# Kernel optimization log

Hardware: AMD Instinct MI355X
Metric: run time of the kernel (lower is better)

## Reference

```python
import jax, jax.numpy as jnp
import numpy as np

HEADS = 16
ROPE_BASE = 10000.0


def _rope(x):
    # x: [B, S, D]; rotate interleaved even/odd pairs across full D
    B, S, D = x.shape
    half = D // 2
    inv_freq = 1.0 / (ROPE_BASE ** (jnp.arange(half, dtype=jnp.float32) * 2.0 / D))
    ang = jnp.arange(S, dtype=jnp.float32)[:, None] * inv_freq[None, :]  # [S, half]
    cos, sin = jnp.cos(ang), jnp.sin(ang)
    xp = x.reshape(B, S, half, 2)
    xe, xo = xp[..., 0], xp[..., 1]
    re = xe * cos - xo * sin
    ro = xe * sin + xo * cos
    return jnp.stack([re, ro], axis=-1).reshape(B, S, D)


def setup_inputs() -> dict:
    key = jax.random.key(0)
    ks = jax.random.split(key, 7)
    B, S, D = 2, 2048, 1024
    sc = 1.0 / np.sqrt(D)
    return {
        "queries": jax.random.normal(ks[0], (B, S, D), jnp.float32),
        "keys": jax.random.normal(ks[1], (B, S, D), jnp.float32),
        "values": jax.random.normal(ks[2], (B, S, D), jnp.float32),
        "Wq": jax.random.normal(ks[3], (D, D), jnp.float32) * sc,
        "Wk": jax.random.normal(ks[4], (D, D), jnp.float32) * sc,
        "Wv": jax.random.normal(ks[5], (D, D), jnp.float32) * sc,
        "Wo": jax.random.normal(ks[6], (D, D), jnp.float32) * sc,
    }


def reference(queries, keys, values, Wq, Wk, Wv, Wo):
    B, S, D = queries.shape
    H = HEADS
    dk = D // H
    # bias-free linear projections (torch Linear: x @ W^T)
    q = _rope(queries @ Wq.T)
    k = _rope(keys @ Wk.T)
    v = _rope(values @ Wv.T)
    # split heads: [B, H, S, dk]
    q = q.reshape(B, S, H, dk).transpose(0, 2, 1, 3)
    k = k.reshape(B, S, H, dk).transpose(0, 2, 1, 3)
    v = v.reshape(B, S, H, dk).transpose(0, 2, 1, 3)
    scores = jnp.einsum("bhqd,bhkd->bhqk", q, k) / jnp.sqrt(jnp.float32(dk))
    attn = jax.nn.softmax(scores, axis=-1)
    ctx = jnp.einsum("bhqk,bhkd->bhqd", attn, v)  # [B, H, S, dk]
    z = ctx.transpose(0, 2, 1, 3).reshape(B, S, D)
    return z @ Wo.T
```

## Files before the change

kernel.cpp:

```cpp
#include <hip/hip_runtime.h>
#include <hip/hip_bf16.h>
#include <math.h>


typedef __attribute__((ext_vector_type(8))) short s8v;
typedef __attribute__((ext_vector_type(8))) __bf16 bf16x8;
typedef __attribute__((ext_vector_type(4))) float f32x4;
typedef __attribute__((ext_vector_type(16))) float f32x16;
typedef __attribute__((ext_vector_type(2))) unsigned u32x2;

__device__ inline unsigned short f2bf(float f) {
    unsigned u = __builtin_bit_cast(unsigned, f);
    u += 0x7FFFu + ((u >> 16) & 1u);
    return (unsigned short)(u >> 16);
}

__device__ inline unsigned pk_bf16(float a, float b) {
    __hip_bfloat162 h = __float22bfloat162_rn(float2{a, b});
    unsigned u;
    __builtin_memcpy(&u, &h, 4);
    return u;
}

__device__ inline f32x4 mfma16(s8v a, s8v b, f32x4 c) {
    return __builtin_amdgcn_mfma_f32_16x16x32_bf16(
        __builtin_bit_cast(bf16x8, a), __builtin_bit_cast(bf16x8, b), c, 0, 0, 0);
}

__device__ inline f32x16 mfma32(s8v a, s8v b, f32x16 c) {
    return __builtin_amdgcn_mfma_f32_32x32x16_bf16(
        __builtin_bit_cast(bf16x8, a), __builtin_bit_cast(bf16x8, b), c, 0, 0, 0);
}

struct CvtArgs {
    const float* s[7];
    unsigned short* d[7];
    int n4[7];
};

__global__ __launch_bounds__(256) void cvt_kernel(CvtArgs a) {
    const int which = blockIdx.y;
    const float4* __restrict__ src = (const float4*)a.s[which];
    unsigned short* __restrict__ dst = a.d[which];
    const int n4 = a.n4[which];
    for (int i = blockIdx.x * 256 + threadIdx.x; i < n4; i += gridDim.x * 256) {
        float4 v = src[i];
        uint2 o;
        o.x = pk_bf16(v.x, v.y);
        o.y = pk_bf16(v.z, v.w);
        *(uint2*)(dst + (size_t)i * 4) = o;
    }
}

__global__ __launch_bounds__(256) void rope_table_kernel(float* __restrict__ cosT,
                                                         float* __restrict__ sinT) {
    int i = blockIdx.x * 256 + threadIdx.x;
    int s = i >> 9, d2 = i & 511;
    float inv = exp2f((float)d2 * (-13.287712379549449f / 512.0f));
    float ang = (float)s * inv;
    float sn, cs;
    sincosf(ang, &sn, &cs);
    cosT[i] = cs;
    sinT[i] = sn;
}

struct GemmArgs {
    const unsigned short* A[3];
    const unsigned short* W[3];
    void* C[3];
    const float* cosT;
    const float* sinT;
    float scale[3];
};

template <bool ROPE>
__global__ __launch_bounds__(256) void gemm_bt(GemmArgs g) {
    constexpr int K = 1024, N = 1024;
    const int z = blockIdx.z;
    const unsigned short* __restrict__ A = g.A[z];
    const unsigned short* __restrict__ W = g.W[z];

    const int tid = threadIdx.x;
    const int lane = tid & 63, wid = tid >> 6;
    const int wr = wid >> 1, wc = wid & 1;
    const int row0 = blockIdx.x * 128, col0 = blockIdx.y * 128;
    const int lr = lane & 15, kofs = (lane >> 4) * 8;

    __shared__ __align__(16) unsigned short As[128][72];
    __shared__ __align__(16) unsigned short Ws[128][72];

    f32x4 acc[4][4] = {};

    const int srow = tid >> 3;
    const int schunk = (tid & 7) * 8;

    for (int k0 = 0; k0 < K; k0 += 64) {
        __syncthreads();
#pragma unroll
        for (int i = 0; i < 4; ++i) {
            int r = srow + i * 32;
            *(s8v*)(&As[r][schunk]) =
                *(const s8v*)(A + (size_t)(row0 + r) * K + k0 + schunk);
            *(s8v*)(&Ws[r][schunk]) =
                *(const s8v*)(W + (size_t)(col0 + r) * K + k0 + schunk);
        }
        __syncthreads();

        s8v af[2][4], bf[2][4];
#pragma unroll
        for (int ks = 0; ks < 2; ++ks) {
#pragma unroll
            for (int m = 0; m < 4; ++m)
                af[ks][m] = *(const s8v*)(&As[wr * 64 + m * 16 + lr][ks * 32 + kofs]);
#pragma unroll
            for (int n = 0; n < 4; ++n)
                bf[ks][n] = *(const s8v*)(&Ws[wc * 64 + n * 16 + lr][ks * 32 + kofs]);
        }
#pragma unroll
        for (int m = 0; m < 4; ++m)
#pragma unroll
            for (int n = 0; n < 4; ++n) {
                acc[m][n] = mfma16(af[0][m], bf[0][n], acc[m][n]);
                acc[m][n] = mfma16(af[1][m], bf[1][n], acc[m][n]);
            }
    }

    const int rbase = row0 + wr * 64 + ((lane >> 4) << 2);
    const int cbase = col0 + wc * 64 + lr;
    const float scale = g.scale[z];
#pragma unroll
    for (int m = 0; m < 4; ++m) {
#pragma unroll
        for (int n = 0; n < 4; ++n) {
            const int gc = cbase + n * 16;
#pragma unroll
            for (int r = 0; r < 4; ++r) {
                const int gr = rbase + m * 16 + r;
                float v = acc[m][n][r];
                if constexpr (ROPE) {
                    const int s = gr & 2047;
                    const int d2 = gc >> 1;
                    float cs = g.cosT[s * 512 + d2];
                    float sn = g.sinT[s * 512 + d2];
                    float partner = __shfl_xor(v, 1);
                    v = (v * cs + partner * ((lane & 1) ? sn : -sn)) * scale;
                    ((unsigned short*)g.C[z])[(size_t)gr * N + gc] = f2bf(v);
                } else {
                    ((float*)g.C[z])[(size_t)gr * N + gc] = v;
                }
            }
        }
    }
}

__global__ __launch_bounds__(512, 2) void attn_kernel(
    const unsigned short* __restrict__ Q,
    const unsigned short* __restrict__ Km,
    const unsigned short* __restrict__ Vm,
    unsigned short* __restrict__ ctx) {
    const int tid = threadIdx.x;
    const int lane = tid & 63;
    const int w = tid >> 6;
    const int hi = lane >> 5;
    const int lq = lane & 31;
    const int qt = blockIdx.x;
    const int bh = blockIdx.y;
    const size_t base = (size_t)(bh >> 4) * 2048 * 1024;
    const int hcol = (bh & 15) * 64;
    const int q0 = qt * 256 + w * 32;

    __shared__ __align__(16) unsigned short Vt[2][64][72];

    const int vkey = tid >> 3;
    const int vc = tid & 7;
    const int vphys = ((((vkey >> 3) ^ vc) << 3) | (vkey & 7));

    auto stageV = [&](int buf, s8v vv) {
#pragma unroll
        for (int j = 0; j < 8; ++j)
            Vt[buf][vc * 8 + j][vphys] = (unsigned short)vv[j];
    };

    const unsigned short* __restrict__ Kp = Km + base + (size_t)lq * 1024 + hcol + hi * 8;
    const unsigned short* __restrict__ Vp = Vm + base + (size_t)vkey * 1024 + hcol + vc * 8;

    s8v qf[4];
#pragma unroll
    for (int s = 0; s < 4; ++s)
        qf[s] = *(const s8v*)(Q + base + (size_t)(q0 + lq) * 1024 + hcol + s * 16 + hi * 8);

    s8v kfA[8], kfB[8];
#pragma unroll
    for (int i = 0; i < 8; ++i)
        kfA[i] = *(const s8v*)(Kp + (size_t)((i >> 2) * 32) * 1024 + (i & 3) * 16);

    stageV(0, *(const s8v*)Vp);
    __syncthreads();

    f32x16 accO0 = {}, accO1 = {};
    float lacc = 0.f;

#define ATTN_STEP(KT, CUR, KFC, KFN)                                            \
    {                                                                           \
        const int kt_ = (KT);                                                   \
        const bool pre_ = (kt_ + 64 < 2048);                                    \
        s8v vnxt_;                                                              \
        if (pre_) {                                                             \
                               \
            vnxt_ = *(const s8v*)(Vp + (size_t)(kt_ + 64) * 1024);              \
            __builtin_amdgcn_sched_barrier(0);                                  \
            _Pragma("unroll")                                                   \
            for (int i = 0; i < 8; ++i)                                         \
                KFN[i] = *(const s8v*)(Kp +                                     \
                    (size_t)(kt_ + 64 + (i >> 2) * 32) * 1024 + (i & 3) * 16);  \
        }                                                                       \
                                       \
        f32x16 s0 = {}, s1 = {};                                                \
        __builtin_amdgcn_s_setprio(1);                                          \
        _Pragma("unroll")                                                       \
        for (int s = 0; s < 4; ++s) {                                           \
            s0 = mfma32(KFC[s], qf[s], s0);                                     \
            s1 = mfma32(KFC[4 + s], qf[s], s1);                                 \
        }                                                                       \
        __builtin_amdgcn_s_setprio(0);                                          \
                                 \
        s8v vf[8];                                                              \
        _Pragma("unroll")                                                       \
        for (int db = 0; db < 2; ++db)                                          \
            _Pragma("unroll")                                                   \
            for (int ks = 0; ks < 4; ++ks)                                      \
                vf[db * 4 + ks] = *(const s8v*)&Vt[CUR][db * 32 + lq]           \
                    [((2 * ks + hi) ^ ((db * 4 + (lq >> 3)) & 7)) << 3];        \
                                  \
        _Pragma("unroll")                                                       \
        for (int r = 0; r < 16; ++r) {                                          \
            s0[r] = exp2f(s0[r]);                                               \
            s1[r] = exp2f(s1[r]);                                               \
        }                                                                       \
        float t16[16];                                                          \
        _Pragma("unroll")                                                       \
        for (int r = 0; r < 16; ++r) t16[r] = s0[r] + s1[r];                    \
        _Pragma("unroll")                                                       \
        for (int r = 0; r < 8; ++r) t16[r] += t16[r + 8];                       \
        _Pragma("unroll")                                                       \
        for (int r = 0; r < 4; ++r) t16[r] += t16[r + 4];                       \
        lacc += (t16[0] + t16[1]) + (t16[2] + t16[3]);                          \
                                                 \
        unsigned w0[8], w1[8];                                                  \
        _Pragma("unroll")                                                       \
        for (int g = 0; g < 4; ++g) {                                           \
            const int rr = g * 4;                                               \
            w0[g] = pk_bf16(s0[rr], s0[rr + 1]);                                \
            w1[g] = pk_bf16(s0[rr + 2], s0[rr + 3]);                            \
        }                                                                       \
        _Pragma("unroll")                                                       \
        for (int g = 4; g < 8; ++g) {                                           \
            const int rr = (g - 4) * 4;                                         \
            w0[g] = pk_bf16(s1[rr], s1[rr + 1]);                                \
            w1[g] = pk_bf16(s1[rr + 2], s1[rr + 3]);                            \
        }                                                                       \
               \
        s8v pf[4];                                                              \
        _Pragma("unroll")                                                       \
        for (int ks = 0; ks < 4; ++ks) {                                        \
            int4 fi;                                                            \
            PK_SWAP(fi, w0[2 * ks], w0[2 * ks + 1], w1[2 * ks], w1[2 * ks + 1]);\
            pf[ks] = __builtin_bit_cast(s8v, fi);                               \
        }                                                                       \
         \
                          \
        if (pre_) stageV((CUR) ^ 1, vnxt_);                                     \
        asm volatile("s_waitcnt lgkmcnt(0)" ::: "memory");                      \
        __builtin_amdgcn_s_barrier();                                           \
        __builtin_amdgcn_sched_barrier(0);                                      \
                                                        \
        __builtin_amdgcn_s_setprio(1);                                          \
        _Pragma("unroll")                                                       \
        for (int ks = 0; ks < 4; ++ks) {                                        \
            accO0 = mfma32(vf[ks], pf[ks], accO0);                              \
            accO1 = mfma32(vf[4 + ks], pf[ks], accO1);                          \
        }                                                                       \
        __builtin_amdgcn_s_setprio(0);                                          \
    }

#if __has_builtin(__builtin_amdgcn_permlane32_swap)
#define PK_SWAP(fi, a0, b0, a1, b1)                                             \
    {                                                                           \
        u32x2 ra_ = __builtin_amdgcn_permlane32_swap((a0), (b0), false, false); \
        u32x2 rb_ = __builtin_amdgcn_permlane32_swap((a1), (b1), false, false); \
        fi.x = (int)ra_[0]; fi.y = (int)rb_[0];                                 \
        fi.z = (int)ra_[1]; fi.w = (int)rb_[1];                                 \
    }
#else
#define PK_SWAP(fi, a0, b0, a1, b1)                                             \
    {                                                                           \
        unsigned own0 = hi ? (b0) : (a0);                                       \
        unsigned own1 = hi ? (b1) : (a1);                                       \
        unsigned snd0 = hi ? (a0) : (b0);                                       \
        unsigned snd1 = hi ? (a1) : (b1);                                       \
        unsigned rcv0 = (unsigned)__shfl_xor((int)snd0, 32);                    \
        unsigned rcv1 = (unsigned)__shfl_xor((int)snd1, 32);                    \
        fi.x = (int)(hi ? rcv0 : own0);                                         \
        fi.y = (int)(hi ? rcv1 : own1);                                         \
        fi.z = (int)(hi ? own0 : rcv0);                                         \
        fi.w = (int)(hi ? own1 : rcv1);                                         \
    }
#endif

    for (int kt = 0; kt < 2048; kt += 128) {
        ATTN_STEP(kt, 0, kfA, kfB);
        ATTN_STEP(kt + 64, 1, kfB, kfA);
    }
#undef ATTN_STEP
#undef PK_SWAP

    const float ltot = lacc + __shfl_xor(lacc, 32);
    const float rl = 1.0f / ltot;
    unsigned short* dst = ctx + base + (size_t)(q0 + lq) * 1024 + hcol;
#pragma unroll
    for (int r = 0; r < 16; ++r) {
        const int d = (r & 3) + 8 * (r >> 2) + 4 * hi;
        dst[d] = f2bf(accO0[r] * rl);
        dst[d + 32] = f2bf(accO1[r] * rl);
    }
}

extern "C" void kernel_launch(void* const* d_in, const int* in_sizes, int n_in,
                              void* d_out, int out_size, void* d_ws, size_t ws_size,
                              hipStream_t stream) {
    char* ws = (char*)d_ws;
    size_t off = 0;
    auto alloc = [&](size_t bytes) {
        void* p = ws + off;
        off += (bytes + 255) & ~(size_t)255;
        return p;
    };

    const size_t XB = (size_t)4096 * 1024 * 2;
    const size_t WB = (size_t)1024 * 1024 * 2;
    const size_t TB = (size_t)2048 * 512 * 4;

    unsigned short* Xb[3];
    for (int i = 0; i < 3; ++i) Xb[i] = (unsigned short*)alloc(XB);
    unsigned short* Wb[4];
    for (int i = 0; i < 4; ++i) Wb[i] = (unsigned short*)alloc(WB);
    unsigned short* Qb = (unsigned short*)alloc(XB);
    unsigned short* Kb = (unsigned short*)alloc(XB);
    unsigned short* Vb = (unsigned short*)alloc(XB);
    float* cosT = (float*)alloc(TB);
    float* sinT = (float*)alloc(TB);
    unsigned short* ctx = Xb[0];

    CvtArgs ca;
    unsigned short* dsts[7] = {Xb[0], Xb[1], Xb[2], Wb[0], Wb[1], Wb[2], Wb[3]};
    for (int i = 0; i < 7; ++i) {
        ca.s[i] = (const float*)d_in[i];
        ca.d[i] = dsts[i];
        ca.n4[i] = in_sizes[i] / 4;
    }
    cvt_kernel<<<dim3(1024, 7), 256, 0, stream>>>(ca);

    rope_table_kernel<<<4096, 256, 0, stream>>>(cosT, sinT);

    GemmArgs gp;
    gp.A[0] = Xb[0]; gp.A[1] = Xb[1]; gp.A[2] = Xb[2];
    gp.W[0] = Wb[0]; gp.W[1] = Wb[1]; gp.W[2] = Wb[2];
    gp.C[0] = Qb;    gp.C[1] = Kb;    gp.C[2] = Vb;
    gp.cosT = cosT;  gp.sinT = sinT;
    gp.scale[0] = 0.125f * 1.4426950408889634f;
    gp.scale[1] = 1.0f;
    gp.scale[2] = 1.0f;
    gemm_bt<true><<<dim3(32, 8, 3), 256, 0, stream>>>(gp);

    attn_kernel<<<dim3(8, 32), 512, 0, stream>>>(Qb, Kb, Vb, ctx);

    GemmArgs go;
    go.A[0] = ctx;   go.A[1] = ctx;   go.A[2] = ctx;
    go.W[0] = Wb[3]; go.W[1] = Wb[3]; go.W[2] = Wb[3];
    go.C[0] = d_out; go.C[1] = d_out; go.C[2] = d_out;
    go.cosT = cosT;  go.sinT = sinT;
    go.scale[0] = 1.0f; go.scale[1] = 1.0f; go.scale[2] = 1.0f;
    gemm_bt<false><<<dim3(32, 8, 1), 256, 0, stream>>>(go);
}
```

Baseline: 180.7 us.

## Split attention over two KV halves and add a combine kernel

Each attention block now processes only half of the key/value sequence, doubling the grid to 512 blocks to fill more compute units. Unnormalized fp32 partial outputs and row sums are written to workspace, and a new combine kernel adds the halves, normalizes and converts to bf16. The block index is remapped to interleave work across the chip. This costs extra global memory traffic for the fp32 partials and an additional kernel launch.

```diff
diff --git a/kernel.cpp b/kernel.cpp
--- a/kernel.cpp
+++ b/kernel.cpp
@@ -157,17 +157,23 @@
     const unsigned short* __restrict__ Q,
     const unsigned short* __restrict__ Km,
     const unsigned short* __restrict__ Vm,
-    unsigned short* __restrict__ ctx) {
+    float* __restrict__ Op,
+    float* __restrict__ Lp) {
     const int tid = threadIdx.x;
     const int lane = tid & 63;
     const int w = tid >> 6;
     const int hi = lane >> 5;
     const int lq = lane & 31;
-    const int qt = blockIdx.x;
-    const int bh = blockIdx.y;
+    const int flat = blockIdx.x;
+    const int vid = (flat & 7) * 64 + (flat >> 3);
+    const int qt = vid & 7;
+    const int bh = (vid >> 3) & 31;
+    const int half = vid >> 8;
     const size_t base = (size_t)(bh >> 4) * 2048 * 1024;
     const int hcol = (bh & 15) * 64;
     const int q0 = qt * 256 + w * 32;
+    const int kv0 = half * 1024;
+    const int kend = kv0 + 1024;
 
     __shared__ __align__(16) unsigned short Vt[2][64][72];
 
@@ -192,9 +198,9 @@
     s8v kfA[8], kfB[8];
 #pragma unroll
     for (int i = 0; i < 8; ++i)
-        kfA[i] = *(const s8v*)(Kp + (size_t)((i >> 2) * 32) * 1024 + (i & 3) * 16);
-
-    stageV(0, *(const s8v*)Vp);
+        kfA[i] = *(const s8v*)(Kp + (size_t)(kv0 + (i >> 2) * 32) * 1024 + (i & 3) * 16);
+
+    stageV(0, *(const s8v*)(Vp + (size_t)kv0 * 1024));
     __syncthreads();
 
     f32x16 accO0 = {}, accO1 = {};
@@ -203,7 +209,7 @@
 #define ATTN_STEP(KT, CUR, KFC, KFN)                                            \
     {                                                                           \
         const int kt_ = (KT);                                                   \
-        const bool pre_ = (kt_ + 64 < 2048);                                    \
+        const bool pre_ = (kt_ + 64 < kend);                                    \
         s8v vnxt_;                                                              \
         if (pre_) {                                                             \
                                \
@@ -267,8 +273,8 @@
             PK_SWAP(fi, w0[2 * ks], w0[2 * ks + 1], w1[2 * ks], w1[2 * ks + 1]);\
             pf[ks] = __builtin_bit_cast(s8v, fi);                               \
         }                                                                       \
-         \
-                          \
+           \
+                      \
         if (pre_) stageV((CUR) ^ 1, vnxt_);                                     \
         asm volatile("s_waitcnt lgkmcnt(0)" ::: "memory");                      \
         __builtin_amdgcn_s_barrier();                                           \
@@ -307,22 +313,43 @@
     }
 #endif
 
-    for (int kt = 0; kt < 2048; kt += 128) {
+    for (int kt = kv0; kt < kend; kt += 128) {
         ATTN_STEP(kt, 0, kfA, kfB);
         ATTN_STEP(kt + 64, 1, kfB, kfA);
     }
 #undef ATTN_STEP
 #undef PK_SWAP
 
+    const int grow = (bh >> 4) * 2048 + q0 + lq;
+    float* dst = Op + ((size_t)half * 4096 + grow) * 1024 + hcol;
+#pragma unroll
+    for (int g = 0; g < 4; ++g) {
+        float4 v0 = make_float4(accO0[g * 4], accO0[g * 4 + 1],
+                                accO0[g * 4 + 2], accO0[g * 4 + 3]);
+        float4 v1 = make_float4(accO1[g * 4], accO1[g * 4 + 1],
+                                accO1[g * 4 + 2], accO1[g * 4 + 3]);
+        *(float4*)(dst + g * 8 + 4 * hi) = v0;
+        *(float4*)(dst + 32 + g * 8 + 4 * hi) = v1;
+    }
     const float ltot = lacc + __shfl_xor(lacc, 32);
-    const float rl = 1.0f / ltot;
-    unsigned short* dst = ctx + base + (size_t)(q0 + lq) * 1024 + hcol;
-#pragma unroll
-    for (int r = 0; r < 16; ++r) {
-        const int d = (r & 3) + 8 * (r >> 2) + 4 * hi;
-        dst[d] = f2bf(accO0[r] * rl);
-        dst[d + 32] = f2bf(accO1[r] * rl);
-    }
+    if (!hi) Lp[((size_t)half * 4096 + grow) * 16 + (bh & 15)] = ltot;
+}
+
+__global__ __launch_bounds__(256) void combine_kernel(const float* __restrict__ Op,
+                                                      const float* __restrict__ Lp,
+                                                      unsigned short* __restrict__ ctx) {
+    const int i = blockIdx.x * 256 + threadIdx.x;
+    const int row = i >> 8;
+    const int h = (i & 255) >> 4;
+    const float l = Lp[row * 16 + h] + Lp[4096 * 16 + row * 16 + h];
+    const float rl = 1.0f / l;
+    const float4* p = (const float4*)Op;
+    float4 a = p[i];
+    float4 b = p[(4096 * 1024 / 4) + i];
+    uint2 o;
+    o.x = pk_bf16((a.x + b.x) * rl, (a.y + b.y) * rl);
+    o.y = pk_bf16((a.z + b.z) * rl, (a.w + b.w) * rl);
+    *(uint2*)(ctx + (size_t)i * 4) = o;
 }
 
 extern "C" void kernel_launch(void* const* d_in, const int* in_sizes, int n_in,
@@ -349,6 +376,8 @@
     unsigned short* Vb = (unsigned short*)alloc(XB);
     float* cosT = (float*)alloc(TB);
     float* sinT = (float*)alloc(TB);
+    float* Op = (float*)alloc((size_t)2 * 4096 * 1024 * 4);
+    float* Lp = (float*)alloc((size_t)2 * 4096 * 16 * 4);
     unsigned short* ctx = Xb[0];
 
     CvtArgs ca;
@@ -372,7 +401,9 @@
     gp.scale[2] = 1.0f;
     gemm_bt<true><<<dim3(32, 8, 3), 256, 0, stream>>>(gp);
 
-    attn_kernel<<<dim3(8, 32), 512, 0, stream>>>(Qb, Kb, Vb, ctx);
+    attn_kernel<<<512, 512, 0, stream>>>(Qb, Kb, Vb, Op, Lp);
+
+    combine_kernel<<<4096, 256, 0, stream>>>(Op, Lp, ctx);
 
     GemmArgs go;
     go.A[0] = ctx;   go.A[1] = ctx;   go.A[2] = ctx;
```

Measured after the change: 190.1 us. 1.05x slower.

## Software-pipeline QK scores one tile ahead and remap attention block order

Applied to the files above, without the earlier changes.

Restructures the attention loop so the QK^T MFMA for the next key tile runs before the exp/softmax and PV of the current tile, with score accumulators ping-ponged and K fragments prefetched two tiles ahead. The V tile in shared memory goes from a 2-deep to a 4-deep ring, and the XOR swizzle is replaced by a padded row stride of 66. The grid is flattened and remapped so that consecutive blocks cover different heads rather than the same head. The aim is to overlap matrix-core work with the exp and pack work and to improve L2 locality. The cost is more live registers, and the unswizzled padded layout may bring back LDS bank conflicts.

```diff
diff --git a/kernel.cpp b/kernel.cpp
--- a/kernel.cpp
+++ b/kernel.cpp
@@ -163,26 +163,22 @@
     const int w = tid >> 6;
     const int hi = lane >> 5;
     const int lq = lane & 31;
-    const int qt = blockIdx.x;
-    const int bh = blockIdx.y;
+    const int flat = blockIdx.x;
+    const int vid = (flat & 7) * 32 + (flat >> 3);
+    const int qt = vid & 7;
+    const int bh = vid >> 3;
     const size_t base = (size_t)(bh >> 4) * 2048 * 1024;
     const int hcol = (bh & 15) * 64;
     const int q0 = qt * 256 + w * 32;
 
-    __shared__ __align__(16) unsigned short Vt[2][64][72];
+    __shared__ __align__(16) unsigned short Vt[4][64][66];
 
     const int vkey = tid >> 3;
     const int vc = tid & 7;
-    const int vphys = ((((vkey >> 3) ^ vc) << 3) | (vkey & 7));
-
-    auto stageV = [&](int buf, s8v vv) {
-#pragma unroll
-        for (int j = 0; j < 8; ++j)
-            Vt[buf][vc * 8 + j][vphys] = (unsigned short)vv[j];
-    };
-
-    const unsigned short* __restrict__ Kp = Km + base + (size_t)lq * 1024 + hcol + hi * 8;
-    const unsigned short* __restrict__ Vp = Vm + base + (size_t)vkey * 1024 + hcol + vc * 8;
+
+    const unsigned short* kpa = Km + base + (size_t)lq * 1024 + hcol + hi * 8;
+    const unsigned short* kpb = kpa + 32 * 1024;
+    const unsigned short* vst = Vm + base + (size_t)vkey * 1024 + hcol + vc * 8;
 
     s8v qf[4];
 #pragma unroll
@@ -192,96 +188,28 @@
     s8v kfA[8], kfB[8];
 #pragma unroll
     for (int i = 0; i < 8; ++i)
-        kfA[i] = *(const s8v*)(Kp + (size_t)((i >> 2) * 32) * 1024 + (i & 3) * 16);
-
-    stageV(0, *(const s8v*)Vp);
+        kfA[i] = *(const s8v*)(((i >> 2) ? kpb : kpa) + (i & 3) * 16);
+    {
+        s8v v0 = *(const s8v*)vst;
+#pragma unroll
+        for (int j = 0; j < 8; ++j) Vt[0][vc * 8 + j][vkey] = (unsigned short)v0[j];
+    }
+#pragma unroll
+    for (int i = 0; i < 8; ++i)
+        kfB[i] = *(const s8v*)(((i >> 2) ? kpb : kpa) + 65536 + (i & 3) * 16);
+    f32x16 scA0 = {}, scA1 = {}, scB0 = {}, scB1 = {};
+#pragma unroll
+    for (int s = 0; s < 4; ++s) {
+        scA0 = mfma32(kfA[s], qf[s], scA0);
+        scA1 = mfma32(kfA[4 + s], qf[s], scA1);
+    }
+    kpa += 2 * 65536;
+    kpb += 2 * 65536;
+    vst += 65536;
     __syncthreads();
 
     f32x16 accO0 = {}, accO1 = {};
     float lacc = 0.f;
-
-#define ATTN_STEP(KT, CUR, KFC, KFN)                                            \
-    {                                                                           \
-        const int kt_ = (KT);                                                   \
-        const bool pre_ = (kt_ + 64 < 2048);                                    \
-        s8v vnxt_;                                                              \
-        if (pre_) {                                                             \
-                               \
-            vnxt_ = *(const s8v*)(Vp + (size_t)(kt_ + 64) * 1024);              \
-            __builtin_amdgcn_sched_barrier(0);                                  \
-            _Pragma("unroll")                                                   \
-            for (int i = 0; i < 8; ++i)                                         \
-                KFN[i] = *(const s8v*)(Kp +                                     \
-                    (size_t)(kt_ + 64 + (i >> 2) * 32) * 1024 + (i & 3) * 16);  \
-        }                                                                       \
-                                       \
-        f32x16 s0 = {}, s1 = {};                                                \
-        __builtin_amdgcn_s_setprio(1);                                          \
-        _Pragma("unroll")                                                       \
-        for (int s = 0; s < 4; ++s) {                                           \
-            s0 = mfma32(KFC[s], qf[s], s0);                                     \
-            s1 = mfma32(KFC[4 + s], qf[s], s1);                                 \
-        }                                                                       \
-        __builtin_amdgcn_s_setprio(0);                                          \
-                                 \
-        s8v vf[8];                                                              \
-        _Pragma("unroll")                                                       \
-        for (int db = 0; db < 2; ++db)                                          \
-            _Pragma("unroll")                                                   \
-            for (int ks = 0; ks < 4; ++ks)                                      \
-                vf[db * 4 + ks] = *(const s8v*)&Vt[CUR][db * 32 + lq]           \
-                    [((2 * ks + hi) ^ ((db * 4 + (lq >> 3)) & 7)) << 3];        \
-                                  \
-        _Pragma("unroll")                                                       \
-        for (int r = 0; r < 16; ++r) {                                          \
-            s0[r] = exp2f(s0[r]);                                               \
-            s1[r] = exp2f(s1[r]);                                               \
-        }                                                                       \
-        float t16[16];                                                          \
-        _Pragma("unroll")                                                       \
-        for (int r = 0; r < 16; ++r) t16[r] = s0[r] + s1[r];                    \
-        _Pragma("unroll")                                                       \
-        for (int r = 0; r < 8; ++r) t16[r] += t16[r + 8];                       \
-        _Pragma("unroll")                                                       \
-        for (int r = 0; r < 4; ++r) t16[r] += t16[r + 4];                       \
-        lacc += (t16[0] + t16[1]) + (t16[2] + t16[3]);                          \
-                                                 \
-        unsigned w0[8], w1[8];                                                  \
-        _Pragma("unroll")                                                       \
-        for (int g = 0; g < 4; ++g) {                                           \
-            const int rr = g * 4;                                               \
-            w0[g] = pk_bf16(s0[rr], s0[rr + 1]);                                \
-            w1[g] = pk_bf16(s0[rr + 2], s0[rr + 3]);                            \
-        }                                                                       \
-        _Pragma("unroll")                                                       \
-        for (int g = 4; g < 8; ++g) {                                           \
-            const int rr = (g - 4) * 4;                                         \
-            w0[g] = pk_bf16(s1[rr], s1[rr + 1]);                                \
-            w1[g] = pk_bf16(s1[rr + 2], s1[rr + 3]);                            \
-        }                                                                       \
-               \
-        s8v pf[4];                                                              \
-        _Pragma("unroll")                                                       \
-        for (int ks = 0; ks < 4; ++ks) {                                        \
-            int4 fi;                                                            \
-            PK_SWAP(fi, w0[2 * ks], w0[2 * ks + 1], w1[2 * ks], w1[2 * ks + 1]);\
-            pf[ks] = __builtin_bit_cast(s8v, fi);                               \
-        }                                                                       \
-         \
-                          \
-        if (pre_) stageV((CUR) ^ 1, vnxt_);                                     \
-        asm volatile("s_waitcnt lgkmcnt(0)" ::: "memory");                      \
-        __builtin_amdgcn_s_barrier();                                           \
-        __builtin_amdgcn_sched_barrier(0);                                      \
-                                                        \
-        __builtin_amdgcn_s_setprio(1);                                          \
-        _Pragma("unroll")                                                       \
-        for (int ks = 0; ks < 4; ++ks) {                                        \
-            accO0 = mfma32(vf[ks], pf[ks], accO0);                              \
-            accO1 = mfma32(vf[4 + ks], pf[ks], accO1);                          \
-        }                                                                       \
-        __builtin_amdgcn_s_setprio(0);                                          \
-    }
 
 #if __has_builtin(__builtin_amdgcn_permlane32_swap)
 #define PK_SWAP(fi, a0, b0, a1, b1)                                             \
@@ -307,11 +235,94 @@
     }
 #endif
 
-    for (int kt = 0; kt < 2048; kt += 128) {
-        ATTN_STEP(kt, 0, kfA, kfB);
-        ATTN_STEP(kt + 64, 1, kfB, kfA);
-    }
-#undef ATTN_STEP
+#define STEP(KT, BC, BN, C0, C1, N0, N1, KFC, KFN)                              \
+    {                                                                           \
+        const int kt_ = (KT);                                                   \
+        const bool h1_ = (kt_ + 64 < 2048);                                     \
+        const bool h2_ = (kt_ + 128 < 2048);                                    \
+        s8v vnxt_;                                                              \
+        if (h1_) vnxt_ = *(const s8v*)vst;                                      \
+        if (h2_) {                                                              \
+            _Pragma("unroll")                                                   \
+            for (int i = 0; i < 8; ++i)                                         \
+                KFN[i] = *(const s8v*)(((i >> 2) ? kpb : kpa) + (i & 3) * 16);  \
+        }                                                                       \
+        __builtin_amdgcn_sched_barrier(0);                                      \
+                   \
+        if (h1_) {                                                              \
+            f32x16 z0 = {}, z1 = {};                                            \
+            __builtin_amdgcn_s_setprio(1);                                      \
+            _Pragma("unroll")                                                   \
+            for (int s = 0; s < 4; ++s) {                                       \
+                z0 = mfma32(KFC[s], qf[s], z0);                                 \
+                z1 = mfma32(KFC[4 + s], qf[s], z1);                             \
+            }                                                                   \
+            __builtin_amdgcn_s_setprio(0);                                      \
+            N0 = z0; N1 = z1;                                                   \
+        }                                                                       \
+                         \
+        _Pragma("unroll")                                                       \
+        for (int r = 0; r < 16; ++r) {                                          \
+            C0[r] = exp2f(C0[r]);                                               \
+            C1[r] = exp2f(C1[r]);                                               \
+        }                                                                       \
+        float t16[16];                                                          \
+        _Pragma("unroll")                                                       \
+        for (int r = 0; r < 16; ++r) t16[r] = C0[r] + C1[r];                    \
+        _Pragma("unroll")                                                       \
+        for (int r = 0; r < 8; ++r) t16[r] += t16[r + 8];                       \
+        _Pragma("unroll")                                                       \
+        for (int r = 0; r < 4; ++r) t16[r] += t16[r + 4];                       \
+        lacc += (t16[0] + t16[1]) + (t16[2] + t16[3]);                          \
+        unsigned w0[8], w1[8];                                                  \
+        _Pragma("unroll")                                                       \
+        for (int g = 0; g < 4; ++g) {                                           \
+            const int rr = g * 4;                                               \
+            w0[g] = pk_bf16(C0[rr], C0[rr + 1]);                                \
+            w1[g] = pk_bf16(C0[rr + 2], C0[rr + 3]);                            \
+        }                                                                       \
+        _Pragma("unroll")                                                       \
+        for (int g = 4; g < 8; ++g) {                                           \
+            const int rr = (g - 4) * 4;                                         \
+            w0[g] = pk_bf16(C1[rr], C1[rr + 1]);                                \
+            w1[g] = pk_bf16(C1[rr + 2], C1[rr + 3]);                            \
+        }                                                                       \
+        s8v pf[4];                                                              \
+        _Pragma("unroll")                                                       \
+        for (int ks = 0; ks < 4; ++ks) {                                        \
+            int4 fi;                                                            \
+            PK_SWAP(fi, w0[2 * ks], w0[2 * ks + 1], w1[2 * ks], w1[2 * ks + 1]);\
+            pf[ks] = __builtin_bit_cast(s8v, fi);                               \
+        }                                                                       \
+              \
+        if (h1_) {                                                              \
+            _Pragma("unroll")                                                   \
+            for (int j = 0; j < 8; ++j)                                         \
+                Vt[BN][vc * 8 + j][vkey] = (unsigned short)vnxt_[j];            \
+        }                                                                       \
+        asm volatile("s_waitcnt lgkmcnt(0)" ::: "memory");                      \
+        __builtin_amdgcn_s_barrier();                                           \
+        __builtin_amdgcn_sched_barrier(0);                                      \
+                                      \
+        __builtin_amdgcn_s_setprio(1);                                          \
+        _Pragma("unroll")                                                       \
+        for (int ks = 0; ks < 4; ++ks) {                                        \
+            s8v vf0 = *(const s8v*)&Vt[BC][lq][ks * 16 + hi * 8];               \
+            s8v vf1 = *(const s8v*)&Vt[BC][32 + lq][ks * 16 + hi * 8];          \
+            accO0 = mfma32(vf0, pf[ks], accO0);                                 \
+            accO1 = mfma32(vf1, pf[ks], accO1);                                 \
+        }                                                                       \
+        __builtin_amdgcn_s_setprio(0);                                          \
+        kpa += 65536; kpb += 65536; vst += 65536;                               \
+    }
+
+    for (int kt0 = 0; kt0 < 2048; kt0 += 256) {
+        STEP(kt0,       0, 1, scA0, scA1, scB0, scB1, kfB, kfA);
+        STEP(kt0 + 64,  1, 2, scB0, scB1, scA0, scA1, kfA, kfB);
+        STEP(kt0 + 128, 2, 3, scA0, scA1, scB0, scB1, kfB, kfA);
+        STEP(kt0 + 192, 3, 0, scB0, scB1, scA0, scA1, kfA, kfB);
+    }
+#undef STEP
 #undef PK_SWAP
 
     const float ltot = lacc + __shfl_xor(lacc, 32);
@@ -372,7 +383,7 @@
     gp.scale[2] = 1.0f;
     gemm_bt<true><<<dim3(32, 8, 3), 256, 0, stream>>>(gp);
 
-    attn_kernel<<<dim3(8, 32), 512, 0, stream>>>(Qb, Kb, Vb, ctx);
+    attn_kernel<<<256, 512, 0, stream>>>(Qb, Kb, Vb, ctx);
 
     GemmArgs go;
     go.A[0] = ctx;   go.A[1] = ctx;   go.A[2] = ctx;
```

New measurement: 207.5 us. 14.8% more time.

## Halve attention block size, remap grid, and drop V LDS swizzle

Applied to the files above, without the earlier changes.

The attention kernel now uses 256-thread blocks covering 128 queries each, launched as a flat 512-block grid. Block indices are remapped so that consecutive blocks are spread across heads. Each thread stages two V rows with a plain padded transpose (row stride 66) in place of the XOR swizzle. V fragments are now read from LDS after the barrier instead of before. The aim is more blocks for better CU occupancy and load balance, at the cost of more K/V reloads per query and possible LDS bank conflicts from the unswizzled layout.

```diff
diff --git a/kernel.cpp b/kernel.cpp
--- a/kernel.cpp
+++ b/kernel.cpp
@@ -153,7 +153,7 @@
     }
 }
 
-__global__ __launch_bounds__(512, 2) void attn_kernel(
+__global__ __launch_bounds__(256, 2) void attn_kernel(
     const unsigned short* __restrict__ Q,
     const unsigned short* __restrict__ Km,
     const unsigned short* __restrict__ Vm,
@@ -163,26 +163,22 @@
     const int w = tid >> 6;
     const int hi = lane >> 5;
     const int lq = lane & 31;
-    const int qt = blockIdx.x;
-    const int bh = blockIdx.y;
+    const int flat = blockIdx.x;
+    const int vid = (flat & 7) * 64 + (flat >> 3);
+    const int qt = vid & 15;
+    const int bh = vid >> 4;
     const size_t base = (size_t)(bh >> 4) * 2048 * 1024;
     const int hcol = (bh & 15) * 64;
-    const int q0 = qt * 256 + w * 32;
-
-    __shared__ __align__(16) unsigned short Vt[2][64][72];
+    const int q0 = qt * 128 + w * 32;
+
+    __shared__ __align__(16) unsigned short Vt[2][64][66];
 
     const int vkey = tid >> 3;
     const int vc = tid & 7;
-    const int vphys = ((((vkey >> 3) ^ vc) << 3) | (vkey & 7));
-
-    auto stageV = [&](int buf, s8v vv) {
-#pragma unroll
-        for (int j = 0; j < 8; ++j)
-            Vt[buf][vc * 8 + j][vphys] = (unsigned short)vv[j];
-    };
-
-    const unsigned short* __restrict__ Kp = Km + base + (size_t)lq * 1024 + hcol + hi * 8;
-    const unsigned short* __restrict__ Vp = Vm + base + (size_t)vkey * 1024 + hcol + vc * 8;
+
+    const unsigned short* kpa = Km + base + (size_t)lq * 1024 + hcol + hi * 8;
+    const unsigned short* kpb = kpa + 32 * 1024;
+    const unsigned short* vst = Vm + base + (size_t)vkey * 1024 + hcol + vc * 8;
 
     s8v qf[4];
 #pragma unroll
@@ -192,96 +188,21 @@
     s8v kfA[8], kfB[8];
 #pragma unroll
     for (int i = 0; i < 8; ++i)
-        kfA[i] = *(const s8v*)(Kp + (size_t)((i >> 2) * 32) * 1024 + (i & 3) * 16);
-
-    stageV(0, *(const s8v*)Vp);
+        kfA[i] = *(const s8v*)(((i >> 2) ? kpb : kpa) + (i & 3) * 16);
+    {
+        s8v v00 = *(const s8v*)vst;
+        s8v v01 = *(const s8v*)(vst + 32 * 1024);
+#pragma unroll
+        for (int j = 0; j < 8; ++j) {
+            Vt[0][vc * 8 + j][vkey] = (unsigned short)v00[j];
+            Vt[0][vc * 8 + j][vkey + 32] = (unsigned short)v01[j];
+        }
+    }
+    kpa += 65536; kpb += 65536; vst += 65536;
     __syncthreads();
 
     f32x16 accO0 = {}, accO1 = {};
     float lacc = 0.f;
-
-#define ATTN_STEP(KT, CUR, KFC, KFN)                                            \
-    {                                                                           \
-        const int kt_ = (KT);                                                   \
-        const bool pre_ = (kt_ + 64 < 2048);                                    \
-        s8v vnxt_;                                                              \
-        if (pre_) {                                                             \
-                               \
-            vnxt_ = *(const s8v*)(Vp + (size_t)(kt_ + 64) * 1024);              \
-            __builtin_amdgcn_sched_barrier(0);                                  \
-            _Pragma("unroll")                                                   \
-            for (int i = 0; i < 8; ++i)                                         \
-                KFN[i] = *(const s8v*)(Kp +                                     \
-                    (size_t)(kt_ + 64 + (i >> 2) * 32) * 1024 + (i & 3) * 16);  \
-        }                                                                       \
-                                       \
-        f32x16 s0 = {}, s1 = {};                                                \
-        __builtin_amdgcn_s_setprio(1);                                          \
-        _Pragma("unroll")                                                       \
-        for (int s = 0; s < 4; ++s) {                                           \
-            s0 = mfma32(KFC[s], qf[s], s0);                                     \
-            s1 = mfma32(KFC[4 + s], qf[s], s1);                                 \
-        }                                                                       \
-        __builtin_amdgcn_s_setprio(0);                                          \
-                                 \
-        s8v vf[8];                                                              \
-        _Pragma("unroll")                                                       \
-        for (int db = 0; db < 2; ++db)                                          \
-            _Pragma("unroll")                                                   \
-            for (int ks = 0; ks < 4; ++ks)                                      \
-                vf[db * 4 + ks] = *(const s8v*)&Vt[CUR][db * 32 + lq]           \
-                    [((2 * ks + hi) ^ ((db * 4 + (lq >> 3)) & 7)) << 3];        \
-                                  \
-        _Pragma("unroll")                                                       \
-        for (int r = 0; r < 16; ++r) {                                          \
-            s0[r] = exp2f(s0[r]);                                               \
-            s1[r] = exp2f(s1[r]);                                               \
-        }                                                                       \
-        float t16[16];                                                          \
-        _Pragma("unroll")                                                       \
-        for (int r = 0; r < 16; ++r) t16[r] = s0[r] + s1[r];                    \
-        _Pragma("unroll")                                                       \
-        for (int r = 0; r < 8; ++r) t16[r] += t16[r + 8];                       \
-        _Pragma("unroll")                                                       \
-        for (int r = 0; r < 4; ++r) t16[r] += t16[r + 4];                       \
-        lacc += (t16[0] + t16[1]) + (t16[2] + t16[3]);                          \
-                                                 \
-        unsigned w0[8], w1[8];                                                  \
-        _Pragma("unroll")                                                       \
-        for (int g = 0; g < 4; ++g) {                                           \
-            const int rr = g * 4;                                               \
-            w0[g] = pk_bf16(s0[rr], s0[rr + 1]);                                \
-            w1[g] = pk_bf16(s0[rr + 2], s0[rr + 3]);                            \
-        }                                                                       \
-        _Pragma("unroll")                                                       \
-        for (int g = 4; g < 8; ++g) {                                           \
-            const int rr = (g - 4) * 4;                                         \
-            w0[g] = pk_bf16(s1[rr], s1[rr + 1]);                                \
-            w1[g] = pk_bf16(s1[rr + 2], s1[rr + 3]);                            \
-        }                                                                       \
-               \
-        s8v pf[4];                                                              \
-        _Pragma("unroll")                                                       \
-        for (int ks = 0; ks < 4; ++ks) {                                        \
-            int4 fi;                                                            \
-            PK_SWAP(fi, w0[2 * ks], w0[2 * ks + 1], w1[2 * ks], w1[2 * ks + 1]);\
-            pf[ks] = __builtin_bit_cast(s8v, fi);                               \
-        }                                                                       \
-         \
-                          \
-        if (pre_) stageV((CUR) ^ 1, vnxt_);                                     \
-        asm volatile("s_waitcnt lgkmcnt(0)" ::: "memory");                      \
-        __builtin_amdgcn_s_barrier();                                           \
-        __builtin_amdgcn_sched_barrier(0);                                      \
-                                                        \
-        __builtin_amdgcn_s_setprio(1);                                          \
-        _Pragma("unroll")                                                       \
-        for (int ks = 0; ks < 4; ++ks) {                                        \
-            accO0 = mfma32(vf[ks], pf[ks], accO0);                              \
-            accO1 = mfma32(vf[4 + ks], pf[ks], accO1);                          \
-        }                                                                       \
-        __builtin_amdgcn_s_setprio(0);                                          \
-    }
 
 #if __has_builtin(__builtin_amdgcn_permlane32_swap)
 #define PK_SWAP(fi, a0, b0, a1, b1)                                             \
@@ -307,6 +228,87 @@
     }
 #endif
 
+#define ATTN_STEP(KT, CUR, KFC, KFN)                                            \
+    {                                                                           \
+        const int kt_ = (KT);                                                   \
+        const bool pre_ = (kt_ + 64 < 2048);                                    \
+        s8v vn0_, vn1_;                                                         \
+        if (pre_) {                                                             \
+              \
+            vn0_ = *(const s8v*)vst;                                            \
+            vn1_ = *(const s8v*)(vst + 32 * 1024);                              \
+            __builtin_amdgcn_sched_barrier(0);                                  \
+            _Pragma("unroll")                                                   \
+            for (int i = 0; i < 8; ++i)                                         \
+                KFN[i] = *(const s8v*)(((i >> 2) ? kpb : kpa) + (i & 3) * 16);  \
+        }                                                                       \
+                                                      \
+        f32x16 s0 = {}, s1 = {};                                                \
+        __builtin_amdgcn_s_setprio(1);                                          \
+        _Pragma("unroll")                                                       \
+        for (int s = 0; s < 4; ++s) {                                           \
+            s0 = mfma32(KFC[s], qf[s], s0);                                     \
+            s1 = mfma32(KFC[4 + s], qf[s], s1);                                 \
+        }                                                                       \
+        __builtin_amdgcn_s_setprio(0);                                          \
+                                  \
+        _Pragma("unroll")                                                       \
+        for (int r = 0; r < 16; ++r) {                                          \
+            s0[r] = exp2f(s0[r]);                                               \
+            s1[r] = exp2f(s1[r]);                                               \
+        }                                                                       \
+        float t16[16];                                                          \
+        _Pragma("unroll")                                                       \
+        for (int r = 0; r < 16; ++r) t16[r] = s0[r] + s1[r];                    \
+        _Pragma("unroll")                                                       \
+        for (int r = 0; r < 8; ++r) t16[r] += t16[r + 8];                       \
+        _Pragma("unroll")                                                       \
+        for (int r = 0; r < 4; ++r) t16[r] += t16[r + 4];                       \
+        lacc += (t16[0] + t16[1]) + (t16[2] + t16[3]);                          \
+        unsigned w0[8], w1[8];                                                  \
+        _Pragma("unroll")                                                       \
+        for (int g = 0; g < 4; ++g) {                                           \
+            const int rr = g * 4;                                               \
+            w0[g] = pk_bf16(s0[rr], s0[rr + 1]);                                \
+            w1[g] = pk_bf16(s0[rr + 2], s0[rr + 3]);                            \
+        }                                                                       \
+        _Pragma("unroll")                                                       \
+        for (int g = 4; g < 8; ++g) {                                           \
+            const int rr = (g - 4) * 4;                                         \
+            w0[g] = pk_bf16(s1[rr], s1[rr + 1]);                                \
+            w1[g] = pk_bf16(s1[rr + 2], s1[rr + 3]);                            \
+        }                                                                       \
+        s8v pf[4];                                                              \
+        _Pragma("unroll")                                                       \
+        for (int ks = 0; ks < 4; ++ks) {                                        \
+            int4 fi;                                                            \
+            PK_SWAP(fi, w0[2 * ks], w0[2 * ks + 1], w1[2 * ks], w1[2 * ks + 1]);\
+            pf[ks] = __builtin_bit_cast(s8v, fi);                               \
+        }                                                                       \
+                      \
+        if (pre_) {                                                             \
+            _Pragma("unroll")                                                   \
+            for (int j = 0; j < 8; ++j) {                                       \
+                Vt[(CUR) ^ 1][vc * 8 + j][vkey] = (unsigned short)vn0_[j];      \
+                Vt[(CUR) ^ 1][vc * 8 + j][vkey + 32] = (unsigned short)vn1_[j]; \
+            }                                                                   \
+        }                                                                       \
+        asm volatile("s_waitcnt lgkmcnt(0)" ::: "memory");                      \
+        __builtin_amdgcn_s_barrier();                                           \
+        __builtin_amdgcn_sched_barrier(0);                                      \
+                                        \
+        __builtin_amdgcn_s_setprio(1);                                          \
+        _Pragma("unroll")                                                       \
+        for (int ks = 0; ks < 4; ++ks) {                                        \
+            s8v vf0 = *(const s8v*)&Vt[CUR][lq][ks * 16 + hi * 8];              \
+            s8v vf1 = *(const s8v*)&Vt[CUR][32 + lq][ks * 16 + hi * 8];         \
+            accO0 = mfma32(vf0, pf[ks], accO0);                                 \
+            accO1 = mfma32(vf1, pf[ks], accO1);                                 \
+        }                                                                       \
+        __builtin_amdgcn_s_setprio(0);                                          \
+        kpa += 65536; kpb += 65536; vst += 65536;                               \
+    }
+
     for (int kt = 0; kt < 2048; kt += 128) {
         ATTN_STEP(kt, 0, kfA, kfB);
         ATTN_STEP(kt + 64, 1, kfB, kfA);
@@ -372,7 +374,7 @@
     gp.scale[2] = 1.0f;
     gemm_bt<true><<<dim3(32, 8, 3), 256, 0, stream>>>(gp);
 
-    attn_kernel<<<dim3(8, 32), 512, 0, stream>>>(Qb, Kb, Vb, ctx);
+    attn_kernel<<<512, 256, 0, stream>>>(Qb, Kb, Vb, ctx);
 
     GemmArgs go;
     go.A[0] = ctx;   go.A[1] = ctx;   go.A[2] = ctx;
```

After: 173.8 us. 1.04x faster.
